# Optimization experiments

Hardware: AMD Instinct MI355X
Metric: run time of the kernel (lower is better)

Reference implementation:

```python
import jax, jax.numpy as jnp
import numpy as np

BN_EPS = 1e-5

def cbr(x, W, g, b, m, v):
    # 1x1 conv (no bias) + folded BatchNorm (inference) + ReLU.
    # x: [B, Cin, H, W], W: [Cout, Cin]
    y = jnp.einsum('bchw,oc->bohw', x, W)
    scale = g * jax.lax.rsqrt(v + BN_EPS)            # [Cout]
    shift = b - m * scale                            # [Cout]
    y = y * scale[None, :, None, None] + shift[None, :, None, None]
    return jax.nn.relu(y)

def setup_inputs() -> dict:
    key = jax.random.key(0)
    ks = iter(jax.random.split(key, 40))
    B, INC, KEYC, H, W, K = 8, 512, 256, 128, 128, 19
    d = {}
    d['x'] = jax.random.normal(next(ks), (B, INC, H, W), jnp.float32)
    d['proxy'] = jax.random.normal(next(ks), (B, INC, K, 1), jnp.float32)
    def wmat(o, i):
        return jax.random.normal(next(ks), (o, i), jnp.float32) * 0.05
    def bnp(c):
        return (jax.random.uniform(next(ks), (c,), jnp.float32),
                jax.random.normal(next(ks), (c,), jnp.float32),
                jax.random.normal(next(ks), (c,), jnp.float32),
                jax.random.uniform(next(ks), (c,), jnp.float32))
    d['pw1'] = wmat(KEYC, INC); d['pg1'], d['pb1'], d['pm1'], d['pv1'] = bnp(KEYC)
    d['pw2'] = wmat(KEYC, KEYC); d['pg2'], d['pb2'], d['pm2'], d['pv2'] = bnp(KEYC)
    d['ow1'] = wmat(KEYC, INC); d['og1'], d['ob1'], d['om1'], d['ov1'] = bnp(KEYC)
    d['ow2'] = wmat(KEYC, KEYC); d['og2'], d['ob2'], d['om2'], d['ov2'] = bnp(KEYC)
    d['dw'] = wmat(KEYC, INC); d['dg'], d['db'], d['dm'], d['dv'] = bnp(KEYC)
    d['uw'] = wmat(INC, KEYC); d['ug'], d['ub'], d['um'], d['uv'] = bnp(INC)
    return d

def reference(x, proxy,
              pw1, pg1, pb1, pm1, pv1, pw2, pg2, pb2, pm2, pv2,
              ow1, og1, ob1, om1, ov1, ow2, og2, ob2, om2, ov2,
              dw, dg, db, dm, dv,
              uw, ug, ub, um, uv):
    B, _, H, W = x.shape
    keyc = pw1.shape[0]
    # f_pixel: two conv1x1+BN+ReLU -> query [B, N, keyc]
    q = cbr(cbr(x, pw1, pg1, pb1, pm1, pv1), pw2, pg2, pb2, pm2, pv2)
    q = q.reshape(B, keyc, H * W).transpose(0, 2, 1)           # [B, N, keyc]
    # f_object -> key [B, keyc, K]
    k = cbr(cbr(proxy, ow1, og1, ob1, om1, ov1), ow2, og2, ob2, om2, ov2)
    k = k.reshape(B, keyc, -1)                                  # [B, keyc, K]
    # f_down -> value [B, K, keyc]
    v = cbr(proxy, dw, dg, db, dm, dv).reshape(B, keyc, -1).transpose(0, 2, 1)
    # scaled attention over K object proxies
    sim = jnp.einsum('bnc,bck->bnk', q, k) * (keyc ** -0.5)     # [B, N, K]
    attn = jax.nn.softmax(sim, axis=-1)
    ctx = jnp.einsum('bnk,bkc->bnc', attn, v)                   # [B, N, keyc]
    ctx = ctx.transpose(0, 2, 1).reshape(B, keyc, H, W)
    # f_up -> [B, inc, H, W]
    return cbr(ctx, uw, ug, ub, um, uv)
```

## Files before the change

kernel.cpp:

```cpp
#include <hip/hip_runtime.h>

typedef unsigned int u32;
typedef unsigned short u16;
typedef __attribute__((ext_vector_type(8))) short bf16x8;
typedef __attribute__((ext_vector_type(4))) float f32x4;

#define DEVI static __device__ __forceinline__

DEVI u16 f2bf(float f) {
    u32 u = __float_as_uint(f);
    u32 r = u + 0x7FFFu + ((u >> 16) & 1u);
    return (u16)(r >> 16);
}
DEVI float bf2f(u16 s) { return __uint_as_float(((u32)s) << 16); }
DEVI void split2(float a, u16& h, u16& l) {
    h = f2bf(a);
    l = f2bf(a - bf2f(h));
}
DEVI int swz(int row) { return (row & 3) ^ ((row >> 2) & 3); }

DEVI void gload16(const void* g, void* l) {
    __builtin_amdgcn_global_load_lds(
        (const __attribute__((address_space(1))) u32*)g,
        (__attribute__((address_space(3))) u32*)l, 16, 0, 0);
}

union U4 { uint4 v; u16 s[8]; };

__global__ __launch_bounds__(256) void pack_w1_kernel(const float* __restrict__ wsrc,
                                                      u16* __restrict__ ph, u16* __restrict__ pl) {
    int i = blockIdx.x * 256 + threadIdx.x;
    int s = i >> 10, rem = i & 1023;
    int rg = rem >> 6, l = rem & 63;
    int row = rg * 16 + (l >> 2);
    int col = s * 32 + (((l & 3) ^ ((l >> 2) & 3) ^ ((l >> 4) & 3)) * 8);
    U4 hh, ll;
#pragma unroll
    for (int e = 0; e < 8; ++e) split2(wsrc[(size_t)row * 512 + col + e], hh.s[e], ll.s[e]);
    *reinterpret_cast<uint4*>(&ph[(size_t)i * 8]) = hh.v;
    *reinterpret_cast<uint4*>(&pl[(size_t)i * 8]) = ll.v;
}
__global__ __launch_bounds__(256) void pack_w2_kernel(const float* __restrict__ wsrc,
                                                      u16* __restrict__ ph, u16* __restrict__ pl) {
    int i = blockIdx.x * 256 + threadIdx.x;
    int w_ = i >> 11, s2 = (i >> 8) & 7, ni = (i >> 6) & 3, l = i & 63;
    int row = w_ * 64 + ni * 16 + (l & 15);
    int col = s2 * 32 + (l >> 4) * 8;
    U4 hh, ll;
#pragma unroll
    for (int e = 0; e < 8; ++e) split2(wsrc[(size_t)row * 256 + col + e], hh.s[e], ll.s[e]);
    *reinterpret_cast<uint4*>(&ph[(size_t)i * 8]) = hh.v;
    *reinterpret_cast<uint4*>(&pl[(size_t)i * 8]) = ll.v;
}
__global__ __launch_bounds__(256) void pack_wu_kernel(const float* __restrict__ wsrc,
                                                      u16* __restrict__ ph, u16* __restrict__ pl) {
    int i = blockIdx.x * 256 + threadIdx.x;
    int o4 = i >> 12, wc = (i >> 11) & 1, s = (i >> 8) & 7, ni = (i >> 6) & 3, l = i & 63;
    int row = o4 * 128 + wc * 64 + ni * 16 + (l & 15);
    int col = s * 32 + (l >> 4) * 8;
    U4 hh, ll;
#pragma unroll
    for (int e = 0; e < 8; ++e) split2(wsrc[(size_t)row * 256 + col + e], hh.s[e], ll.s[e]);
    *reinterpret_cast<uint4*>(&ph[(size_t)i * 8]) = hh.v;
    *reinterpret_cast<uint4*>(&pl[(size_t)i * 8]) = ll.v;
}

struct KVArgs {
    const float *proxy;
    const float *ow1, *og1, *ob1, *om1, *ov1;
    const float *ow2, *og2, *ob2, *om2, *ov2;
    const float *dw,  *dg,  *db,  *dm,  *dv;
    float *kmat;
    float *vmat;
};
__global__ __launch_bounds__(256) void kv_kernel(KVArgs a) {
    __shared__ float pl[512 * 19];
    __shared__ float t1[256 * 19];
    const int t = threadIdx.x;
    const int b = blockIdx.x;
    const float* pb = a.proxy + (size_t)b * 512 * 19;
    for (int i = t; i < 512 * 19; i += 256) pl[i] = pb[i];
    __syncthreads();
    const int o = t;
    {
        float acc[19] = {0.f};
        const float* wr = a.ow1 + (size_t)o * 512;
        for (int c = 0; c < 512; ++c) {
            float wv = wr[c];
#pragma unroll
            for (int kk = 0; kk < 19; ++kk) acc[kk] += wv * pl[c * 19 + kk];
        }
        float sc = a.og1[o] * __frsqrt_rn(a.ov1[o] + 1e-5f);
        float sh = a.ob1[o] - a.om1[o] * sc;
#pragma unroll
        for (int kk = 0; kk < 19; ++kk) t1[o * 19 + kk] = fmaxf(acc[kk] * sc + sh, 0.f);
    }
    __syncthreads();
    {
        float acc[19] = {0.f};
        const float* wr = a.ow2 + (size_t)o * 256;
        for (int c = 0; c < 256; ++c) {
            float wv = wr[c];
#pragma unroll
            for (int kk = 0; kk < 19; ++kk) acc[kk] += wv * t1[c * 19 + kk];
        }
        float sc = a.og2[o] * __frsqrt_rn(a.ov2[o] + 1e-5f);
        float sh = a.ob2[o] - a.om2[o] * sc;
#pragma unroll
        for (int kk = 0; kk < 19; ++kk)
            a.kmat[((size_t)b * 256 + o) * 19 + kk] = fmaxf(acc[kk] * sc + sh, 0.f);
    }
    {
        float acc[19] = {0.f};
        const float* wr = a.dw + (size_t)o * 512;
        for (int c = 0; c < 512; ++c) {
            float wv = wr[c];
#pragma unroll
            for (int kk = 0; kk < 19; ++kk) acc[kk] += wv * pl[c * 19 + kk];
        }
        float sc = a.dg[o] * __frsqrt_rn(a.dv[o] + 1e-5f);
        float sh = a.db[o] - a.dm[o] * sc;
#pragma unroll
        for (int kk = 0; kk < 19; ++kk)
            a.vmat[((size_t)b * 19 + kk) * 256 + o] = fmaxf(acc[kk] * sc + sh, 0.f);
    }
}

struct AttnArgs { const float* q2f; const float* kmat; const float* vmat;
                  u16* ctxh; u16* ctxl; long long p_off; };
__global__ __launch_bounds__(256, 3) void attn_kernel(AttnArgs a) {
    __shared__ float kl[4864];
    __shared__ float vl[4864];
    __shared__ float sp[128 * 21];
    const int t = threadIdx.x;
    const int px = t & 127, hf = t >> 7;
    const size_t pl_ = (size_t)blockIdx.x * 128;
    const size_t gpx0 = (size_t)a.p_off + pl_;
    const int b = (int)(gpx0 >> 14);
    for (int i = t; i < 4864; i += 256) { kl[i] = a.kmat[(size_t)b * 4864 + i];
                                          vl[i] = a.vmat[(size_t)b * 4864 + i]; }
    __syncthreads();
    const float* qrow = a.q2f + (pl_ + px) * 256 + hf * 128;
    float sim[19];
#pragma unroll
    for (int kk = 0; kk < 19; ++kk) sim[kk] = 0.f;
    for (int j = 0; j < 32; ++j) {
        float4 qv = reinterpret_cast<const float4*>(qrow)[j];
#pragma unroll
        for (int e = 0; e < 4; ++e) {
            float qf = (e == 0) ? qv.x : (e == 1) ? qv.y : (e == 2) ? qv.z : qv.w;
            int c = hf * 128 + j * 4 + e;
#pragma unroll
            for (int kk = 0; kk < 19; ++kk) sim[kk] += qf * kl[c * 19 + kk];
        }
    }
    if (hf == 1) {
#pragma unroll
        for (int kk = 0; kk < 19; ++kk) sp[px * 21 + kk] = sim[kk];
    }
    __syncthreads();
    if (hf == 0) {
        float mx = -1e30f;
#pragma unroll
        for (int kk = 0; kk < 19; ++kk) {
            sim[kk] = (sim[kk] + sp[px * 21 + kk]) * 0.0625f;
            mx = fmaxf(mx, sim[kk]);
        }
        float ssum = 0.f;
#pragma unroll
        for (int kk = 0; kk < 19; ++kk) { sim[kk] = __expf(sim[kk] - mx); ssum += sim[kk]; }
        const float inv = 1.f / ssum;
#pragma unroll
        for (int kk = 0; kk < 19; ++kk) sp[px * 21 + kk] = sim[kk] * inv;
    }
    __syncthreads();
    float wgt[19];
#pragma unroll
    for (int kk = 0; kk < 19; ++kk) wgt[kk] = sp[px * 21 + kk];
    const int Pg = (int)(gpx0) + px;
    const int tile = Pg >> 6, r = Pg & 63;
    const int pgg = r >> 4, l15a = r & 15;
    u16* th = a.ctxh + (size_t)tile * 16384;
    u16* tl = a.ctxl + (size_t)tile * 16384;
#pragma unroll
    for (int j2 = 0; j2 < 16; ++j2) {
        const int j = hf * 16 + j2;
        const int s = j >> 2, l4c = j & 3;
        U4 hh, ll;
#pragma unroll
        for (int e = 0; e < 8; ++e) {
            int c = j * 8 + e;
            float acc = 0.f;
#pragma unroll
            for (int kk = 0; kk < 19; ++kk) acc += wgt[kk] * vl[kk * 256 + c];
            split2(acc, hh.s[e], ll.s[e]);
        }
        const int off = (s * 4 + pgg) * 512 + (l4c * 16 + l15a) * 8;
        *reinterpret_cast<uint4*>(&th[off]) = hh.v;
        *reinterpret_cast<uint4*>(&tl[off]) = ll.v;
    }
}

struct F12Args {
    const float* Xf;
    const u16 *W1h, *W1l, *W2h, *W2l;
    const float *g1, *b1, *m1, *v1;
    const float *g2, *b2, *m2, *v2;
    float* q2f;
    int m_off;
};
__global__ __launch_bounds__(256, 2) void fused12_kernel(F12Args a) {
    __shared__ char LB[81920];
    u16* xs = (u16*)LB;
    u16* wb = (u16*)(LB + 16384);
    u16* q1 = (u16*)LB;
    float* tf = (float*)LB;

    const int t = threadIdx.x;
    const int l = t & 63, w = t >> 6;
    const int wr = w >> 1, wc = w & 1;
    const int l15 = l & 15, l4 = l >> 4;
    const int mloc = blockIdx.x * 64;
    const int mg = a.m_off + mloc;
    const int bb = mg >> 14, nb = mg & 16383;

    f32x4 acc1[2][8];
#pragma unroll
    for (int mi = 0; mi < 2; ++mi)
#pragma unroll
        for (int ni = 0; ni < 8; ++ni) acc1[mi][ni] = f32x4{0.f, 0.f, 0.f, 0.f};

    float fx[8];

    auto loadX = [&](int s) {
        const int px = t & 63, oct = t >> 6;
        const float* src = a.Xf + (((size_t)bb * 512 + s * 32 + oct * 8) << 14) + nb + px;
#pragma unroll
        for (int e = 0; e < 8; ++e) fx[e] = src[(size_t)e << 14];
    };
    auto writeX = [&](int buf) {
        const int px = t & 63, oct = t >> 6;
        U4 ph, plo;
#pragma unroll
        for (int e = 0; e < 8; ++e) split2(fx[e], ph.s[e], plo.s[e]);
        int pos = buf * 4096 + px * 32 + ((oct ^ swz(px)) * 8);
        *reinterpret_cast<uint4*>(&xs[pos]) = ph.v;
        *reinterpret_cast<uint4*>(&xs[2048 + pos]) = plo.v;
    };
    auto dmaW1 = [&](int s, int buf) {
        const u16* bh = a.W1h + (size_t)s * 8192 + l * 8;
        const u16* bl2 = a.W1l + (size_t)s * 8192 + l * 8;
#pragma unroll
        for (int g = 0; g < 4; ++g) {
            const int rg = w * 4 + g;
            gload16(bh + rg * 512, &wb[buf * 16384 + rg * 512]);
            gload16(bl2 + rg * 512, &wb[buf * 16384 + 8192 + rg * 512]);
        }
    };

    loadX(0); dmaW1(0, 0);
    writeX(0);
    loadX(1);
    __syncthreads();
    int cur = 0;
    for (int s = 0; s < 16; ++s) {
        if (s < 15) dmaW1(s + 1, cur ^ 1);
        bf16x8 ah[2], am[2];
#pragma unroll
        for (int mi = 0; mi < 2; ++mi) {
            int ar = wr * 32 + mi * 16 + l15;
            int ap = cur * 4096 + ar * 32 + ((l4 ^ swz(ar)) * 8);
            ah[mi] = *reinterpret_cast<const bf16x8*>(&xs[ap]);
            am[mi] = *reinterpret_cast<const bf16x8*>(&xs[2048 + ap]);
        }
#pragma unroll
        for (int ni = 0; ni < 8; ++ni) {
            int br = wc * 128 + ni * 16 + l15;
            int bp = cur * 16384 + br * 32 + ((l4 ^ swz(br)) * 8);
            bf16x8 bh = *reinterpret_cast<const bf16x8*>(&wb[bp]);
            bf16x8 bl_ = *reinterpret_cast<const bf16x8*>(&wb[8192 + bp]);
#pragma unroll
            for (int mi = 0; mi < 2; ++mi) {
                acc1[mi][ni] = __builtin_amdgcn_mfma_f32_16x16x32_bf16(ah[mi], bh, acc1[mi][ni], 0, 0, 0);
                acc1[mi][ni] = __builtin_amdgcn_mfma_f32_16x16x32_bf16(ah[mi], bl_, acc1[mi][ni], 0, 0, 0);
                acc1[mi][ni] = __builtin_amdgcn_mfma_f32_16x16x32_bf16(am[mi], bh, acc1[mi][ni], 0, 0, 0);
            }
        }
        if (s < 15) {
            writeX(cur ^ 1);
            if (s < 14) loadX(s + 2);
        }
        __syncthreads();
        cur ^= 1;
    }

    float scl1[8], shf1[8];
#pragma unroll
    for (int ni = 0; ni < 8; ++ni) {
        int o = wc * 128 + ni * 16 + l15;
        scl1[ni] = a.g1[o] * __frsqrt_rn(a.v1[o] + 1e-5f);
        shf1[ni] = a.b1[o] - a.m1[o] * scl1[ni];
    }
    float scl2[4], shf2[4];
#pragma unroll
    for (int ni = 0; ni < 4; ++ni) {
        int o = w * 64 + ni * 16 + l15;
        scl2[ni] = a.g2[o] * __frsqrt_rn(a.v2[o] + 1e-5f);
        shf2[ni] = a.b2[o] - a.m2[o] * scl2[ni];
    }

#pragma unroll
    for (int pxq = 0; pxq < 4; ++pxq) {
        const int mi = pxq & 1;
        __syncthreads();
        if (wr == (pxq >> 1)) {
#pragma unroll
            for (int ni = 0; ni < 8; ++ni) {
                int o1 = wc * 128 + ni * 16 + l15;
                int base = (o1 >> 3) * 8 + (o1 & 7);
#pragma unroll
                for (int r = 0; r < 4; ++r) {
                    int px_l = l4 * 4 + r;
                    float y = fmaxf(acc1[mi][ni][r] * scl1[ni] + shf1[ni], 0.f);
                    u16 h, lo; split2(y, h, lo);
                    int pos = px_l * 280 + base;
                    q1[pos] = h;
                    q1[4480 + pos] = lo;
                }
            }
        }
        __syncthreads();

        f32x4 acc2[4];
#pragma unroll
        for (int ni = 0; ni < 4; ++ni) acc2[ni] = f32x4{0.f, 0.f, 0.f, 0.f};

#pragma unroll
        for (int s2 = 0; s2 < 8; ++s2) {
            int ap = l15 * 280 + (s2 * 4 + l4) * 8;
            bf16x8 a2h = *reinterpret_cast<const bf16x8*>(&q1[ap]);
            bf16x8 a2m = *reinterpret_cast<const bf16x8*>(&q1[4480 + ap]);
            const size_t bo0 = (size_t)(w * 8 + s2) * 2048 + l * 8;
#pragma unroll
            for (int ni = 0; ni < 4; ++ni) {
                bf16x8 b2h = *reinterpret_cast<const bf16x8*>(&a.W2h[bo0 + ni * 512]);
                bf16x8 b2l = *reinterpret_cast<const bf16x8*>(&a.W2l[bo0 + ni * 512]);
                acc2[ni] = __builtin_amdgcn_mfma_f32_16x16x32_bf16(a2h, b2h, acc2[ni], 0, 0, 0);
                acc2[ni] = __builtin_amdgcn_mfma_f32_16x16x32_bf16(a2h, b2l, acc2[ni], 0, 0, 0);
                acc2[ni] = __builtin_amdgcn_mfma_f32_16x16x32_bf16(a2m, b2h, acc2[ni], 0, 0, 0);
            }
        }
        __syncthreads();

#pragma unroll
        for (int ni = 0; ni < 4; ++ni) {
            int o2 = w * 64 + ni * 16 + l15;
#pragma unroll
            for (int r = 0; r < 4; ++r) {
                int px_l = l4 * 4 + r;
                tf[px_l * 260 + o2] = fmaxf(acc2[ni][r] * scl2[ni] + shf2[ni], 0.f);
            }
        }
        __syncthreads();
#pragma unroll
        for (int j = 0; j < 4; ++j) {
            int task = j * 256 + t;
            int row = task >> 6, c4 = task & 63;
            *reinterpret_cast<float4*>(&a.q2f[(size_t)(mloc + pxq * 16 + row) * 256 + c4 * 4]) =
                *reinterpret_cast<const float4*>(&tf[row * 260 + c4 * 4]);
        }
    }
}

struct GUArgs {
    const u16 *Ah, *Al, *Wh, *Wl;
    const float *gg, *bbv, *mmv, *vvv;
    float* Yf;
};
__global__ __launch_bounds__(256, 4) void gemm_up_kernel(GUArgs a) {
    __shared__ float ldsf[128 * 68];
    const int t = threadIdx.x;
    const int l = t & 63;
    const int w = t >> 6;
    const int wr = w >> 1, wc = w & 1;
    const int l15 = l & 15, l4 = l >> 4;
    const int id = blockIdx.y * 4 + blockIdx.x;
    const int wid = (id & 7) * 1024 + (id >> 3);
    const int o0 = (wid & 3) * 128;
    const int m  = (wid >> 2) * 64;
    const int bb = m >> 14;
    const int nb = m & 16383;

    f32x4 acc[2][4];
#pragma unroll
    for (int mi = 0; mi < 2; ++mi)
#pragma unroll
        for (int ni = 0; ni < 4; ++ni) acc[mi][ni] = f32x4{0.f, 0.f, 0.f, 0.f};

    const size_t aoff0 = (size_t)(wid >> 2) * 16384 + (size_t)(wr * 2) * 512 + l * 8;
    const size_t woff0 = (size_t)(((wid & 3) * 2 + wc) * 8) * 2048 + l * 8;

#pragma unroll 2
    for (int s = 0; s < 8; ++s) {
        const size_t as = aoff0 + (size_t)s * 2048;
        const size_t wso = woff0 + (size_t)s * 2048;
        bf16x8 ah[2], al[2], bh[4], bl[4];
#pragma unroll
        for (int mi = 0; mi < 2; ++mi) {
            ah[mi] = *reinterpret_cast<const bf16x8*>(a.Ah + as + mi * 512);
            al[mi] = *reinterpret_cast<const bf16x8*>(a.Al + as + mi * 512);
        }
#pragma unroll
        for (int ni = 0; ni < 4; ++ni) {
            bh[ni] = *reinterpret_cast<const bf16x8*>(a.Wh + wso + ni * 512);
            bl[ni] = *reinterpret_cast<const bf16x8*>(a.Wl + wso + ni * 512);
        }
#pragma unroll
        for (int mi = 0; mi < 2; ++mi)
#pragma unroll
            for (int ni = 0; ni < 4; ++ni) {
                acc[mi][ni] = __builtin_amdgcn_mfma_f32_16x16x32_bf16(ah[mi], bh[ni], acc[mi][ni], 0, 0, 0);
                acc[mi][ni] = __builtin_amdgcn_mfma_f32_16x16x32_bf16(ah[mi], bl[ni], acc[mi][ni], 0, 0, 0);
                acc[mi][ni] = __builtin_amdgcn_mfma_f32_16x16x32_bf16(al[mi], bh[ni], acc[mi][ni], 0, 0, 0);
            }
    }

    float scl[4], shf[4];
#pragma unroll
    for (int ni = 0; ni < 4; ++ni) {
        int o = o0 + wc * 64 + ni * 16 + l15;
        scl[ni] = a.gg[o] * __frsqrt_rn(a.vvv[o] + 1e-5f);
        shf[ni] = a.bbv[o] - a.mmv[o] * scl[ni];
    }

#pragma unroll
    for (int ni = 0; ni < 4; ++ni) {
        int o_l = wc * 64 + ni * 16 + l15;
#pragma unroll
        for (int mi = 0; mi < 2; ++mi)
#pragma unroll
            for (int r = 0; r < 4; ++r) {
                int n_l = wr * 32 + mi * 16 + l4 * 4 + r;
                float y = fmaxf(acc[mi][ni][r] * scl[ni] + shf[ni], 0.f);
                ldsf[o_l * 68 + n_l] = y;
            }
    }
    __syncthreads();
#pragma unroll
    for (int j = 0; j < 8; ++j) {
        int idx = j * 256 + t;
        int row = idx >> 4, c4 = (idx & 15) * 4;
        *reinterpret_cast<float4*>(&a.Yf[((size_t)bb << 23) + (size_t)(o0 + row) * 16384 + nb + c4]) =
            *reinterpret_cast<const float4*>(&ldsf[row * 68 + c4]);
    }
}

extern "C" void kernel_launch(void* const* d_in, const int* in_sizes, int n_in,
                              void* d_out, int out_size, void* d_ws, size_t ws_size,
                              hipStream_t stream) {
    const float* x     = (const float*)d_in[0];
    const float* proxy = (const float*)d_in[1];
    const float* pw1 = (const float*)d_in[2];
    const float* pg1 = (const float*)d_in[3];
    const float* pb1 = (const float*)d_in[4];
    const float* pm1 = (const float*)d_in[5];
    const float* pv1 = (const float*)d_in[6];
    const float* pw2 = (const float*)d_in[7];
    const float* pg2 = (const float*)d_in[8];
    const float* pb2 = (const float*)d_in[9];
    const float* pm2 = (const float*)d_in[10];
    const float* pv2 = (const float*)d_in[11];
    const float* ow1 = (const float*)d_in[12];
    const float* og1 = (const float*)d_in[13];
    const float* ob1 = (const float*)d_in[14];
    const float* om1 = (const float*)d_in[15];
    const float* ov1 = (const float*)d_in[16];
    const float* ow2 = (const float*)d_in[17];
    const float* og2 = (const float*)d_in[18];
    const float* ob2 = (const float*)d_in[19];
    const float* om2 = (const float*)d_in[20];
    const float* ov2 = (const float*)d_in[21];
    const float* dw  = (const float*)d_in[22];
    const float* dg  = (const float*)d_in[23];
    const float* db  = (const float*)d_in[24];
    const float* dm  = (const float*)d_in[25];
    const float* dv  = (const float*)d_in[26];
    const float* uw  = (const float*)d_in[27];
    const float* ug  = (const float*)d_in[28];
    const float* ub  = (const float*)d_in[29];
    const float* um  = (const float*)d_in[30];
    const float* uv  = (const float*)d_in[31];

    char* ws = (char*)d_ws;
    u16* w1ph = (u16*)(ws + 0);
    u16* w1pl = (u16*)(ws + 262144);
    u16* w2ph = (u16*)(ws + 524288);
    u16* w2pl = (u16*)(ws + 655360);
    u16* wuph = (u16*)(ws + 786432);
    u16* wupl = (u16*)(ws + 1048576);
    float* kmat = (float*)(ws + 1310720);
    float* vmat = (float*)(ws + 1466368);
    u16* ctxh = (u16*)(ws + 2097152);
    u16* ctxl = (u16*)(ws + 69206016);
    float* q2f = (float*)(ws + 136314880ull);

    int passes = 1;
    while (passes < 16 && 136314880ull + 134217728ull / (size_t)passes > ws_size) passes <<= 1;

    pack_w1_kernel<<<64, 256, 0, stream>>>(pw1, w1ph, w1pl);
    pack_w2_kernel<<<32, 256, 0, stream>>>(pw2, w2ph, w2pl);
    pack_wu_kernel<<<64, 256, 0, stream>>>(uw,  wuph, wupl);

    KVArgs ka{proxy, ow1, og1, ob1, om1, ov1, ow2, og2, ob2, om2, ov2,
              dw, dg, db, dm, dv, kmat, vmat};
    kv_kernel<<<8, 256, 0, stream>>>(ka);

    const int mpix = 131072 / passes;
    for (int p = 0; p < passes; ++p) {
        const int m_off = p * mpix;
        F12Args fa{x, w1ph, w1pl, w2ph, w2pl,
                   pg1, pb1, pm1, pv1, pg2, pb2, pm2, pv2, q2f, m_off};
        fused12_kernel<<<mpix / 64, 256, 0, stream>>>(fa);
        AttnArgs aa{q2f, kmat, vmat, ctxh, ctxl, (long long)m_off};
        attn_kernel<<<mpix / 128, 256, 0, stream>>>(aa);
    }

    GUArgs ga{ctxh, ctxl, wuph, wupl, ug, ub, um, uv, (float*)d_out};
    gemm_up_kernel<<<dim3(4, 2048), 256, 0, stream>>>(ga);
}
```

Before: 608.1 us.

## Widen fused conv tile to 128 pixels, restructure attention, drop pass loop

The fused two-conv kernel now computes 128 pixels per block instead of 64, which halves how often each W1 tile is fetched, and single-buffers the X tile behind an extra barrier. The attention kernel now handles 16 pixels per block, stages q in shared memory, splits channels across 16 thread groups and reduces partial sums with shuffles plus a shared-memory pass. The workspace-driven multi-pass loop is removed and both kernels are launched once over all pixels. In exchange there are more registers, fewer resident blocks per CU (attention drops to 2), less overlap of X loads with compute, and a q2f buffer that must now hold every pixel whatever the workspace size.

```diff
diff --git a/kernel.cpp b/kernel.cpp
--- a/kernel.cpp
+++ b/kernel.cpp
@@ -128,63 +128,73 @@
 
 struct AttnArgs { const float* q2f; const float* kmat; const float* vmat;
                   u16* ctxh; u16* ctxl; long long p_off; };
-__global__ __launch_bounds__(256, 3) void attn_kernel(AttnArgs a) {
+__global__ __launch_bounds__(256, 2) void attn_kernel(AttnArgs a) {
+    __shared__ float qs[16 * 261];
     __shared__ float kl[4864];
     __shared__ float vl[4864];
-    __shared__ float sp[128 * 21];
+    __shared__ float sp[4 * 16 * 19];
     const int t = threadIdx.x;
-    const int px = t & 127, hf = t >> 7;
-    const size_t pl_ = (size_t)blockIdx.x * 128;
+    const int px = t & 15, cg = t >> 4;
+    const int w = t >> 6, l = t & 63;
+    const size_t pl_ = (size_t)blockIdx.x * 16;
     const size_t gpx0 = (size_t)a.p_off + pl_;
     const int b = (int)(gpx0 >> 14);
     for (int i = t; i < 4864; i += 256) { kl[i] = a.kmat[(size_t)b * 4864 + i];
                                           vl[i] = a.vmat[(size_t)b * 4864 + i]; }
+    {
+        const float* src = a.q2f + pl_ * 256;
+#pragma unroll
+        for (int j = 0; j < 4; ++j) {
+            int f = j * 256 + t;
+            float4 v = reinterpret_cast<const float4*>(src)[f];
+            int pr = f >> 6, col = (f & 63) * 4;
+            *reinterpret_cast<float4*>(&qs[pr * 261 + col]) = v;
+        }
+    }
     __syncthreads();
-    const float* qrow = a.q2f + (pl_ + px) * 256 + hf * 128;
     float sim[19];
 #pragma unroll
     for (int kk = 0; kk < 19; ++kk) sim[kk] = 0.f;
-    for (int j = 0; j < 32; ++j) {
-        float4 qv = reinterpret_cast<const float4*>(qrow)[j];
-#pragma unroll
-        for (int e = 0; e < 4; ++e) {
-            float qf = (e == 0) ? qv.x : (e == 1) ? qv.y : (e == 2) ? qv.z : qv.w;
-            int c = hf * 128 + j * 4 + e;
-#pragma unroll
-            for (int kk = 0; kk < 19; ++kk) sim[kk] += qf * kl[c * 19 + kk];
-        }
-    }
-    if (hf == 1) {
-#pragma unroll
-        for (int kk = 0; kk < 19; ++kk) sp[px * 21 + kk] = sim[kk];
-    }
-    __syncthreads();
-    if (hf == 0) {
-        float mx = -1e30f;
-#pragma unroll
-        for (int kk = 0; kk < 19; ++kk) {
-            sim[kk] = (sim[kk] + sp[px * 21 + kk]) * 0.0625f;
-            mx = fmaxf(mx, sim[kk]);
-        }
-        float ssum = 0.f;
-#pragma unroll
-        for (int kk = 0; kk < 19; ++kk) { sim[kk] = __expf(sim[kk] - mx); ssum += sim[kk]; }
-        const float inv = 1.f / ssum;
-#pragma unroll
-        for (int kk = 0; kk < 19; ++kk) sp[px * 21 + kk] = sim[kk] * inv;
+#pragma unroll 4
+    for (int i = 0; i < 16; ++i) {
+        int c = cg * 16 + i;
+        float qv = qs[px * 261 + c];
+#pragma unroll
+        for (int kk = 0; kk < 19; ++kk) sim[kk] += qv * kl[c * 19 + kk];
+    }
+#pragma unroll
+    for (int kk = 0; kk < 19; ++kk) {
+        sim[kk] += __shfl_xor(sim[kk], 16);
+        sim[kk] += __shfl_xor(sim[kk], 32);
+    }
+    if ((l >> 4) == 0) {
+#pragma unroll
+        for (int kk = 0; kk < 19; ++kk) sp[w * 304 + px * 19 + kk] = sim[kk];
     }
     __syncthreads();
     float wgt[19];
-#pragma unroll
-    for (int kk = 0; kk < 19; ++kk) wgt[kk] = sp[px * 21 + kk];
-    const int Pg = (int)(gpx0) + px;
-    const int tile = Pg >> 6, r = Pg & 63;
-    const int pgg = r >> 4, l15a = r & 15;
+    float mx = -1e30f;
+#pragma unroll
+    for (int kk = 0; kk < 19; ++kk) {
+        float s0 = sp[px * 19 + kk] + sp[304 + px * 19 + kk]
+                 + sp[608 + px * 19 + kk] + sp[912 + px * 19 + kk];
+        wgt[kk] = s0 * 0.0625f;
+        mx = fmaxf(mx, wgt[kk]);
+    }
+    float ssum = 0.f;
+#pragma unroll
+    for (int kk = 0; kk < 19; ++kk) { wgt[kk] = __expf(wgt[kk] - mx); ssum += wgt[kk]; }
+    const float inv = 1.f / ssum;
+#pragma unroll
+    for (int kk = 0; kk < 19; ++kk) wgt[kk] *= inv;
+    const int Pg = (int)gpx0 + px;
+    const int tile = Pg >> 6;
+    const int pgg = (Pg >> 4) & 3;
     u16* th = a.ctxh + (size_t)tile * 16384;
     u16* tl = a.ctxl + (size_t)tile * 16384;
 #pragma unroll
-    for (int j2 = 0; j2 < 16; ++j2) {
-        const int j = hf * 16 + j2;
+    for (int jj = 0; jj < 2; ++jj) {
+        const int j = cg * 2 + jj;
         const int s = j >> 2, l4c = j & 3;
         U4 hh, ll;
 #pragma unroll
@@ -195,7 +205,7 @@
             for (int kk = 0; kk < 19; ++kk) acc += wgt[kk] * vl[kk * 256 + c];
             split2(acc, hh.s[e], ll.s[e]);
         }
-        const int off = (s * 4 + pgg) * 512 + (l4c * 16 + l15a) * 8;
+        const int off = (s * 4 + pgg) * 512 + (l4c * 16 + px) * 8;
         *reinterpret_cast<uint4*>(&th[off]) = hh.v;
         *reinterpret_cast<uint4*>(&tl[off]) = ll.v;
     }
@@ -220,32 +230,37 @@
     const int l = t & 63, w = t >> 6;
     const int wr = w >> 1, wc = w & 1;
     const int l15 = l & 15, l4 = l >> 4;
-    const int mloc = blockIdx.x * 64;
+    const int mloc = blockIdx.x * 128;
     const int mg = a.m_off + mloc;
     const int bb = mg >> 14, nb = mg & 16383;
 
-    f32x4 acc1[2][8];
-#pragma unroll
-    for (int mi = 0; mi < 2; ++mi)
+    f32x4 acc1[4][8];
+#pragma unroll
+    for (int mi = 0; mi < 4; ++mi)
 #pragma unroll
         for (int ni = 0; ni < 8; ++ni) acc1[mi][ni] = f32x4{0.f, 0.f, 0.f, 0.f};
 
-    float fx[8];
+    float fxA[8], fxB[8];
 
     auto loadX = [&](int s) {
-        const int px = t & 63, oct = t >> 6;
-        const float* src = a.Xf + (((size_t)bb * 512 + s * 32 + oct * 8) << 14) + nb + px;
-#pragma unroll
-        for (int e = 0; e < 8; ++e) fx[e] = src[(size_t)e << 14];
+        const int px = t & 127, oa = t >> 7;
+        const float* s0 = a.Xf + (((size_t)bb * 512 + s * 32 + oa * 8) << 14) + nb + px;
+        const float* s1 = a.Xf + (((size_t)bb * 512 + s * 32 + (oa + 2) * 8) << 14) + nb + px;
+#pragma unroll
+        for (int e = 0; e < 8; ++e) { fxA[e] = s0[(size_t)e << 14]; fxB[e] = s1[(size_t)e << 14]; }
     };
-    auto writeX = [&](int buf) {
-        const int px = t & 63, oct = t >> 6;
-        U4 ph, plo;
-#pragma unroll
-        for (int e = 0; e < 8; ++e) split2(fx[e], ph.s[e], plo.s[e]);
-        int pos = buf * 4096 + px * 32 + ((oct ^ swz(px)) * 8);
-        *reinterpret_cast<uint4*>(&xs[pos]) = ph.v;
-        *reinterpret_cast<uint4*>(&xs[2048 + pos]) = plo.v;
+    auto writeX = [&]() {
+        const int px = t & 127, oa = t >> 7;
+        U4 phA, plA, phB, plB;
+#pragma unroll
+        for (int e = 0; e < 8; ++e) { split2(fxA[e], phA.s[e], plA.s[e]);
+                                      split2(fxB[e], phB.s[e], plB.s[e]); }
+        int posA = px * 32 + ((oa ^ swz(px)) * 8);
+        int posB = px * 32 + (((oa + 2) ^ swz(px)) * 8);
+        *reinterpret_cast<uint4*>(&xs[posA]) = phA.v;
+        *reinterpret_cast<uint4*>(&xs[4096 + posA]) = plA.v;
+        *reinterpret_cast<uint4*>(&xs[posB]) = phB.v;
+        *reinterpret_cast<uint4*>(&xs[4096 + posB]) = plB.v;
     };
     auto dmaW1 = [&](int s, int buf) {
         const u16* bh = a.W1h + (size_t)s * 8192 + l * 8;
@@ -259,19 +274,18 @@
     };
 
     loadX(0); dmaW1(0, 0);
-    writeX(0);
-    loadX(1);
+    writeX();
     __syncthreads();
     int cur = 0;
     for (int s = 0; s < 16; ++s) {
         if (s < 15) dmaW1(s + 1, cur ^ 1);
-        bf16x8 ah[2], am[2];
-#pragma unroll
-        for (int mi = 0; mi < 2; ++mi) {
-            int ar = wr * 32 + mi * 16 + l15;
-            int ap = cur * 4096 + ar * 32 + ((l4 ^ swz(ar)) * 8);
+        bf16x8 ah[4], am[4];
+#pragma unroll
+        for (int mi = 0; mi < 4; ++mi) {
+            int ar = wr * 64 + mi * 16 + l15;
+            int ap = ar * 32 + ((l4 ^ swz(ar)) * 8);
             ah[mi] = *reinterpret_cast<const bf16x8*>(&xs[ap]);
-            am[mi] = *reinterpret_cast<const bf16x8*>(&xs[2048 + ap]);
+            am[mi] = *reinterpret_cast<const bf16x8*>(&xs[4096 + ap]);
         }
 #pragma unroll
         for (int ni = 0; ni < 8; ++ni) {
@@ -280,17 +294,18 @@
             bf16x8 bh = *reinterpret_cast<const bf16x8*>(&wb[bp]);
             bf16x8 bl_ = *reinterpret_cast<const bf16x8*>(&wb[8192 + bp]);
 #pragma unroll
-            for (int mi = 0; mi < 2; ++mi) {
+            for (int mi = 0; mi < 4; ++mi) {
                 acc1[mi][ni] = __builtin_amdgcn_mfma_f32_16x16x32_bf16(ah[mi], bh, acc1[mi][ni], 0, 0, 0);
                 acc1[mi][ni] = __builtin_amdgcn_mfma_f32_16x16x32_bf16(ah[mi], bl_, acc1[mi][ni], 0, 0, 0);
                 acc1[mi][ni] = __builtin_amdgcn_mfma_f32_16x16x32_bf16(am[mi], bh, acc1[mi][ni], 0, 0, 0);
             }
         }
+        __syncthreads();
         if (s < 15) {
-            writeX(cur ^ 1);
-            if (s < 14) loadX(s + 2);
-        }
-        __syncthreads();
+            loadX(s + 1);
+            writeX();
+            __syncthreads();
+        }
         cur ^= 1;
     }
 
@@ -310,63 +325,71 @@
     }
 
 #pragma unroll
-    for (int pxq = 0; pxq < 4; ++pxq) {
-        const int mi = pxq & 1;
+    for (int cp = 0; cp < 4; ++cp) {
         __syncthreads();
-        if (wr == (pxq >> 1)) {
-#pragma unroll
-            for (int ni = 0; ni < 8; ++ni) {
-                int o1 = wc * 128 + ni * 16 + l15;
-                int base = (o1 >> 3) * 8 + (o1 & 7);
-#pragma unroll
-                for (int r = 0; r < 4; ++r) {
-                    int px_l = l4 * 4 + r;
-                    float y = fmaxf(acc1[mi][ni][r] * scl1[ni] + shf1[ni], 0.f);
-                    u16 h, lo; split2(y, h, lo);
-                    int pos = px_l * 280 + base;
-                    q1[pos] = h;
-                    q1[4480 + pos] = lo;
-                }
+#pragma unroll
+        for (int ni = 0; ni < 8; ++ni) {
+            int o1 = wc * 128 + ni * 16 + l15;
+#pragma unroll
+            for (int r = 0; r < 4; ++r) {
+                int row = wr * 16 + l4 * 4 + r;
+                float y = fmaxf(acc1[cp][ni][r] * scl1[ni] + shf1[ni], 0.f);
+                u16 h, lo; split2(y, h, lo);
+                int pos = row * 280 + o1;
+                q1[pos] = h;
+                q1[8960 + pos] = lo;
             }
         }
         __syncthreads();
 
-        f32x4 acc2[4];
-#pragma unroll
-        for (int ni = 0; ni < 4; ++ni) acc2[ni] = f32x4{0.f, 0.f, 0.f, 0.f};
+        f32x4 acc2[2][4];
+#pragma unroll
+        for (int m = 0; m < 2; ++m)
+#pragma unroll
+            for (int ni = 0; ni < 4; ++ni) acc2[m][ni] = f32x4{0.f, 0.f, 0.f, 0.f};
 
 #pragma unroll
         for (int s2 = 0; s2 < 8; ++s2) {
-            int ap = l15 * 280 + (s2 * 4 + l4) * 8;
-            bf16x8 a2h = *reinterpret_cast<const bf16x8*>(&q1[ap]);
-            bf16x8 a2m = *reinterpret_cast<const bf16x8*>(&q1[4480 + ap]);
+            bf16x8 a2h[2], a2m[2];
+#pragma unroll
+            for (int m = 0; m < 2; ++m) {
+                int ap = (m * 16 + l15) * 280 + (s2 * 4 + l4) * 8;
+                a2h[m] = *reinterpret_cast<const bf16x8*>(&q1[ap]);
+                a2m[m] = *reinterpret_cast<const bf16x8*>(&q1[8960 + ap]);
+            }
             const size_t bo0 = (size_t)(w * 8 + s2) * 2048 + l * 8;
 #pragma unroll
             for (int ni = 0; ni < 4; ++ni) {
                 bf16x8 b2h = *reinterpret_cast<const bf16x8*>(&a.W2h[bo0 + ni * 512]);
                 bf16x8 b2l = *reinterpret_cast<const bf16x8*>(&a.W2l[bo0 + ni * 512]);
-                acc2[ni] = __builtin_amdgcn_mfma_f32_16x16x32_bf16(a2h, b2h, acc2[ni], 0, 0, 0);
-                acc2[ni] = __builtin_amdgcn_mfma_f32_16x16x32_bf16(a2h, b2l, acc2[ni], 0, 0, 0);
-                acc2[ni] = __builtin_amdgcn_mfma_f32_16x16x32_bf16(a2m, b2h, acc2[ni], 0, 0, 0);
+#pragma unroll
+                for (int m = 0; m < 2; ++m) {
+                    acc2[m][ni] = __builtin_amdgcn_mfma_f32_16x16x32_bf16(a2h[m], b2h, acc2[m][ni], 0, 0, 0);
+                    acc2[m][ni] = __builtin_amdgcn_mfma_f32_16x16x32_bf16(a2h[m], b2l, acc2[m][ni], 0, 0, 0);
+                    acc2[m][ni] = __builtin_amdgcn_mfma_f32_16x16x32_bf16(a2m[m], b2h, acc2[m][ni], 0, 0, 0);
+                }
             }
         }
         __syncthreads();
 
 #pragma unroll
-        for (int ni = 0; ni < 4; ++ni) {
-            int o2 = w * 64 + ni * 16 + l15;
-#pragma unroll
-            for (int r = 0; r < 4; ++r) {
-                int px_l = l4 * 4 + r;
-                tf[px_l * 260 + o2] = fmaxf(acc2[ni][r] * scl2[ni] + shf2[ni], 0.f);
-            }
-        }
+        for (int m = 0; m < 2; ++m)
+#pragma unroll
+            for (int ni = 0; ni < 4; ++ni) {
+                int o2 = w * 64 + ni * 16 + l15;
+#pragma unroll
+                for (int r = 0; r < 4; ++r) {
+                    int row = m * 16 + l4 * 4 + r;
+                    tf[row * 260 + o2] = fmaxf(acc2[m][ni][r] * scl2[ni] + shf2[ni], 0.f);
+                }
+            }
         __syncthreads();
 #pragma unroll
-        for (int j = 0; j < 4; ++j) {
+        for (int j = 0; j < 8; ++j) {
             int task = j * 256 + t;
             int row = task >> 6, c4 = task & 63;
-            *reinterpret_cast<float4*>(&a.q2f[(size_t)(mloc + pxq * 16 + row) * 256 + c4 * 4]) =
+            int gpx = mloc + (row >> 4) * 64 + cp * 16 + (row & 15);
+            *reinterpret_cast<float4*>(&a.q2f[(size_t)gpx * 256 + c4 * 4]) =
                 *reinterpret_cast<const float4*>(&tf[row * 260 + c4 * 4]);
         }
     }
@@ -504,9 +527,6 @@
     u16* ctxl = (u16*)(ws + 69206016);
     float* q2f = (float*)(ws + 136314880ull);
 
-    int passes = 1;
-    while (passes < 16 && 136314880ull + 134217728ull / (size_t)passes > ws_size) passes <<= 1;
-
     pack_w1_kernel<<<64, 256, 0, stream>>>(pw1, w1ph, w1pl);
     pack_w2_kernel<<<32, 256, 0, stream>>>(pw2, w2ph, w2pl);
     pack_wu_kernel<<<64, 256, 0, stream>>>(uw,  wuph, wupl);
@@ -515,15 +535,12 @@
               dw, dg, db, dm, dv, kmat, vmat};
     kv_kernel<<<8, 256, 0, stream>>>(ka);
 
-    const int mpix = 131072 / passes;
-    for (int p = 0; p < passes; ++p) {
-        const int m_off = p * mpix;
-        F12Args fa{x, w1ph, w1pl, w2ph, w2pl,
-                   pg1, pb1, pm1, pv1, pg2, pb2, pm2, pv2, q2f, m_off};
-        fused12_kernel<<<mpix / 64, 256, 0, stream>>>(fa);
-        AttnArgs aa{q2f, kmat, vmat, ctxh, ctxl, (long long)m_off};
-        attn_kernel<<<mpix / 128, 256, 0, stream>>>(aa);
-    }
+    F12Args fa{x, w1ph, w1pl, w2ph, w2pl,
+               pg1, pb1, pm1, pv1, pg2, pb2, pm2, pv2, q2f, 0};
+    fused12_kernel<<<1024, 256, 0, stream>>>(fa);
+
+    AttnArgs aa{q2f, kmat, vmat, ctxh, ctxl, 0};
+    attn_kernel<<<8192, 256, 0, stream>>>(aa);
 
     GUArgs ga{ctxh, ctxl, wuph, wupl, ug, ub, um, uv, (float*)d_out};
     gemm_up_kernel<<<dim3(4, 2048), 256, 0, stream>>>(ga);
```

After: 609.4 us. No clear change (+0.2%).
